# Kernel tuning notes

Hardware: AMD Instinct MI355X
Metric: run time of the kernel (lower is better)

Reference implementation:

```python
import jax, jax.numpy as jnp
import numpy as np

TOP_K = 1024  # init top_k


def setup_inputs() -> dict:
    key = jax.random.key(0)
    ks = jax.random.split(key, 11)
    B, S, D, H = 8, 1024, 1024, 4096
    s = 0.02
    return {
        "inputs": jax.random.normal(ks[0], (B, S, D), jnp.float32),
        "up_w": jax.random.normal(ks[1], (H, D), jnp.float32) * s,
        "up_b": jax.random.normal(ks[2], (H,), jnp.float32) * s,
        "gate_w1": jax.random.normal(ks[3], (H, D), jnp.float32) * s,
        "gate_b1": jax.random.normal(ks[4], (H,), jnp.float32) * s,
        "gate_w2": jax.random.normal(ks[5], (H, H), jnp.float32) * s,
        "gate_b2": jax.random.normal(ks[6], (H,), jnp.float32) * s,
        "mod_w": jax.random.normal(ks[7], (H, D), jnp.float32) * s,
        "mod_b": jax.random.normal(ks[8], (H,), jnp.float32) * s,
        "down_w": jax.random.normal(ks[9], (D, H), jnp.float32) * s,
        "down_b": jax.random.normal(ks[10], (D,), jnp.float32) * s,
    }


def reference(inputs, up_w, up_b, gate_w1, gate_b1, gate_w2, gate_b2,
              mod_w, mod_b, down_w, down_b):
    B, S, D = inputs.shape
    H = up_w.shape[0]
    # gate: Linear -> ReLU -> Linear, scores [B,S,H]
    scores = jax.nn.relu(jnp.einsum('bsd,hd->bsh', inputs, gate_w1) + gate_b1)
    scores = jnp.einsum('bsh,gh->bsg', scores, gate_w2) + gate_b2
    flat_scores = scores.reshape(B, S * H)
    k = min(TOP_K * S, S * H)
    _, flat_idx = jax.lax.top_k(flat_scores, k)          # [B,k]
    hidden_idx = flat_idx % H                            # [B,k]
    # scatter writes mod.weight[h] at row h -> duplicates harmless -> boolean mask
    batch_idx = jnp.broadcast_to(jnp.arange(B)[:, None], (B, k))
    mask = jnp.zeros((B, H), bool).at[batch_idx, hidden_idx].set(True)
    # per-batch modified weights/bias (materialized like torch repeat+index_put)
    w = jnp.where(mask[:, :, None], mod_w[None], up_w[None])   # [B,H,D]
    b = jnp.where(mask, mod_b[None], up_b[None])               # [B,H]
    h = jnp.einsum('bsd,bhd->bsh', inputs, w) + b[:, None, :]
    h = jax.nn.silu(h)
    # dropout p=0.0 (eval) -> identity
    return jnp.einsum('bsh,dh->bsd', h, down_w) + down_b
```

## Files before the change

kernel.cpp:

```cpp
#include <hip/hip_runtime.h>
#include <cstdint>

typedef __attribute__((ext_vector_type(8))) short short8;
typedef __attribute__((ext_vector_type(4))) float floatx4;
typedef unsigned int uint32;

typedef const void __attribute__((address_space(1)))* gcptr;
typedef void __attribute__((address_space(3)))* lptr;

constexpr int Bn = 8, Sn = 1024, Dn = 1024, Hn = 4096;
constexpr uint32 KTOP = 1024u * 1024u;
constexpr uint32 SKBASE = 0xBB000000u;
constexpr uint32 EMAX = (1u << 27) - 1u;
constexpr uint32 WLO = 3645;
constexpr uint32 WHI = 4157;
constexpr uint32 CAP = 1u << 20;

constexpr size_t NX  = (size_t)Bn * Sn * Dn;
constexpr size_t NW1 = (size_t)Hn * Dn;
constexpr size_t NW2 = (size_t)Hn * Hn;
constexpr size_t NRS = (size_t)Bn * Sn * Hn;

constexpr size_t OFF_XH   = 0;
constexpr size_t OFF_XL   = OFF_XH  + 2 * NX;
constexpr size_t OFF_W1H  = OFF_XL  + 2 * NX;
constexpr size_t OFF_W1L  = OFF_W1H + 2 * NW1;
constexpr size_t OFF_W2H  = OFF_W1L + 2 * NW1;
constexpr size_t OFF_W2L  = OFF_W2H + 2 * NW2;
constexpr size_t OFF_RSH  = OFF_W2L + 2 * NW2;
constexpr size_t OFF_RSL  = OFF_RSH + 2 * NRS;
constexpr size_t OFF_HIST = OFF_RSL + 2 * NRS;
constexpr size_t OFF_HIST2= OFF_HIST + (size_t)Bn * 8192 * 4;
constexpr size_t OFF_HMAX = OFF_HIST2+ (size_t)Bn * 16384 * 4;
constexpr size_t OFF_META = OFF_HMAX + (size_t)Bn * Hn * 4;
constexpr size_t OFF_BSEL = OFF_META + 4096;
constexpr size_t OFF_MASK = OFF_BSEL + (size_t)Bn * Hn * 4;
constexpr size_t WS_SMALL = OFF_MASK + (size_t)Bn * Hn * 4;
constexpr size_t ZERO_BYTES = OFF_BSEL - OFF_HIST;
constexpr size_t OFF_BUF  = OFF_XL;

__device__ __forceinline__ ushort f2bf(float f) {
  uint32 u = __float_as_uint(f);
  u += 0x7fffu + ((u >> 16) & 1u);
  return (ushort)(u >> 16);
}
__device__ __forceinline__ float bf2f(ushort h) {
  return __uint_as_float(((uint32)h) << 16);
}
__device__ __forceinline__ uint32 skey(float v) {
  uint32 u = __float_as_uint(v);
  return (u & 0x80000000u) ? ~u : (u | 0x80000000u);
}
__device__ __forceinline__ uint32 ekey(uint32 key) {
  if (key <= SKBASE) return 0u;
  uint32 d = key - SKBASE;
  return d > EMAX ? EMAX : d;
}
__device__ __forceinline__ void g2l(const ushort* src, ushort* dst) {
  __builtin_amdgcn_global_load_lds((gcptr)src, (lptr)dst, 16, 0, 0);
}
__device__ __forceinline__ void stage_tile(ushort* lds, const ushort* gbase, int ldg, int tid) {
  const int w = tid >> 6;
  const int c0 = tid, c1 = tid + 256;
  g2l(gbase + (size_t)(c0 >> 2) * ldg + (c0 & 3) * 8, lds + (size_t)(w * 64) * 8);
  g2l(gbase + (size_t)(c1 >> 2) * ldg + (c1 & 3) * 8, lds + (size_t)(256 + w * 64) * 8);
}
__device__ __forceinline__ void stage_tile_sel(ushort* lds, const ushort* upw,
                                               const ushort* modw, const uint32* bm,
                                               int n0, int k0, int ldg, int tid) {
  const int w = tid >> 6;
  const int c0 = tid, c1 = tid + 256;
  const int r0 = n0 + (c0 >> 2), r1 = n0 + (c1 >> 2);
  const ushort* s0 = (bm[r0] ? modw : upw) + (size_t)r0 * ldg + k0 + (c0 & 3) * 8;
  const ushort* s1 = (bm[r1] ? modw : upw) + (size_t)r1 * ldg + k0 + (c1 & 3) * 8;
  g2l(s0, lds + (size_t)(w * 64) * 8);
  g2l(s1, lds + (size_t)(256 + w * 64) * 8);
}

__global__ __launch_bounds__(256) void cvt_split_k(const float4* __restrict__ x,
                                                   ushort* __restrict__ hi,
                                                   ushort* __restrict__ lo, int n4) {
  int stride = gridDim.x * 256;
  for (int i = blockIdx.x * 256 + threadIdx.x; i < n4; i += stride) {
    float4 v = x[i];
    ushort h0 = f2bf(v.x), h1 = f2bf(v.y), h2 = f2bf(v.z), h3 = f2bf(v.w);
    ushort4 hv; hv.x = h0; hv.y = h1; hv.z = h2; hv.w = h3;
    *(ushort4*)(hi + (size_t)i * 4) = hv;
    ushort4 lv;
    lv.x = f2bf(v.x - bf2f(h0)); lv.y = f2bf(v.y - bf2f(h1));
    lv.z = f2bf(v.z - bf2f(h2)); lv.w = f2bf(v.w - bf2f(h3));
    *(ushort4*)(lo + (size_t)i * 4) = lv;
  }
}
__global__ __launch_bounds__(256) void cvt_single_k(const float4* __restrict__ x,
                                                    ushort* __restrict__ hi, int n4) {
  int stride = gridDim.x * 256;
  for (int i = blockIdx.x * 256 + threadIdx.x; i < n4; i += stride) {
    float4 v = x[i];
    ushort4 hv; hv.x = f2bf(v.x); hv.y = f2bf(v.y); hv.z = f2bf(v.z); hv.w = f2bf(v.w);
    *(ushort4*)(hi + (size_t)i * 4) = hv;
  }
}
__global__ __launch_bounds__(256) void zero_out_k(float* __restrict__ o, int n) {
  int i = blockIdx.x * 256 + threadIdx.x;
  if (i < n) o[i] = 0.f;
}

constexpr int EPI_RELU = 0;
constexpr int EPI_SCORE = 1;
constexpr int EPI_SILU = 2;
constexpr int EPI_F32 = 3;

template <bool SPLIT, bool SELB, int EPI>
__global__ __launch_bounds__(256, SPLIT ? 3 : 2) void gemm_bt(
    const ushort* __restrict__ Ah, const ushort* __restrict__ Al,
    const ushort* __restrict__ Bh, const ushort* __restrict__ Bl,
    const uint32* __restrict__ bmask,
    int N, int K, long long a_bs, long long o_bs, long long bias_bs,
    const float* __restrict__ bias,
    void* __restrict__ outp, void* __restrict__ out2p,
    uint32* __restrict__ hist, uint32* __restrict__ hmax,
    uint32* __restrict__ buf, uint32* __restrict__ cnt) {
  static_assert(EPI != EPI_SCORE || SPLIT, "score path is split");
  __shared__ __align__(16) ushort lds[SPLIT ? 16384 : 8192];
  ushort* As = lds;
  ushort* Bs = lds + (SPLIT ? 8192 : 4096);

  const int tid = threadIdx.x;
  const int w = tid >> 6, l = tid & 63;
  const int wm = (w >> 1) << 6, wn = (w & 1) << 6;
  const int lm = l & 15, lq = l >> 4;
  const int m0 = blockIdx.y << 7, n0 = blockIdx.x << 7;
  const int z = blockIdx.z;

  const ushort* pAh = Ah + (size_t)z * a_bs + (size_t)m0 * K;
  const ushort* pAl = SPLIT ? Al + (size_t)z * a_bs + (size_t)m0 * K : nullptr;
  const ushort* pBh = SELB ? nullptr : Bh + (size_t)n0 * K;
  const ushort* pBl = (SPLIT && !SELB) ? Bl + (size_t)n0 * K : nullptr;
  const uint32* bm = SELB ? bmask + (size_t)z * Hn : nullptr;

  floatx4 acc[4][4];
#pragma unroll
  for (int i = 0; i < 4; i++)
#pragma unroll
    for (int j = 0; j < 4; j++) acc[i][j] = floatx4{0.f, 0.f, 0.f, 0.f};

  for (int k0 = 0; k0 < K; k0 += 32) {
    stage_tile(As, pAh + k0, K, tid);
    if constexpr (SELB)
      stage_tile_sel(Bs, Bh, Bl, bm, n0, k0, K, tid);
    else
      stage_tile(Bs, pBh + k0, K, tid);
    if constexpr (SPLIT) {
      stage_tile(As + 4096, pAl + k0, K, tid);
      stage_tile(Bs + 4096, pBl + k0, K, tid);
    }
    __syncthreads();
    short8 afh[4], bfh[4];
#pragma unroll
    for (int i = 0; i < 4; i++)
      afh[i] = *(const short8*)&As[(wm + i * 16 + lm) * 32 + lq * 8];
#pragma unroll
    for (int i = 0; i < 4; i++)
      bfh[i] = *(const short8*)&Bs[(wn + i * 16 + lm) * 32 + lq * 8];
#pragma unroll
    for (int mi = 0; mi < 4; mi++)
#pragma unroll
      for (int ni = 0; ni < 4; ni++)
        acc[mi][ni] = __builtin_amdgcn_mfma_f32_16x16x32_bf16(afh[mi], bfh[ni], acc[mi][ni], 0, 0, 0);
    if constexpr (SPLIT) {
      {
        short8 afl[4];
#pragma unroll
        for (int i = 0; i < 4; i++)
          afl[i] = *(const short8*)&As[4096 + (wm + i * 16 + lm) * 32 + lq * 8];
#pragma unroll
        for (int mi = 0; mi < 4; mi++)
#pragma unroll
          for (int ni = 0; ni < 4; ni++)
            acc[mi][ni] = __builtin_amdgcn_mfma_f32_16x16x32_bf16(afl[mi], bfh[ni], acc[mi][ni], 0, 0, 0);
      }
      {
        short8 bfl[4];
#pragma unroll
        for (int i = 0; i < 4; i++)
          bfl[i] = *(const short8*)&Bs[4096 + (wn + i * 16 + lm) * 32 + lq * 8];
#pragma unroll
        for (int mi = 0; mi < 4; mi++)
#pragma unroll
          for (int ni = 0; ni < 4; ni++)
            acc[mi][ni] = __builtin_amdgcn_mfma_f32_16x16x32_bf16(afh[mi], bfl[ni], acc[mi][ni], 0, 0, 0);
      }
    }
    __syncthreads();
  }

  if constexpr (EPI == EPI_RELU) {
    ushort* rh = (ushort*)outp;
    ushort* rl = (ushort*)out2p;
#pragma unroll
    for (int mi = 0; mi < 4; mi++)
#pragma unroll
      for (int ni = 0; ni < 4; ni++) {
        int gm = m0 + wm + mi * 16 + lq * 4;
        int gn = n0 + wn + ni * 16 + lm;
        float bnv = bias[gn];
#pragma unroll
        for (int r = 0; r < 4; r++) {
          float v = fmaxf(acc[mi][ni][r] + bnv, 0.f);
          ushort h = f2bf(v);
          size_t o = (size_t)(gm + r) * N + gn;
          rh[o] = h;
          rl[o] = f2bf(v - bf2f(h));
        }
      }
  } else if constexpr (EPI == EPI_SILU) {
    ushort* o = (ushort*)outp + (size_t)z * o_bs;
    const float* bb = bias + (size_t)z * bias_bs;
#pragma unroll
    for (int mi = 0; mi < 4; mi++)
#pragma unroll
      for (int ni = 0; ni < 4; ni++) {
        int gm = m0 + wm + mi * 16 + lq * 4;
        int gn = n0 + wn + ni * 16 + lm;
        float bnv = bb[gn];
#pragma unroll
        for (int r = 0; r < 4; r++) {
          float v = acc[mi][ni][r] + bnv;
          float s = v / (1.f + __expf(-v));
          o[(size_t)(gm + r) * N + gn] = f2bf(s);
        }
      }
  } else if constexpr (EPI == EPI_F32) {
    float* o = (float*)outp;
#pragma unroll
    for (int mi = 0; mi < 4; mi++)
#pragma unroll
      for (int ni = 0; ni < 4; ni++) {
        int gm = m0 + wm + mi * 16 + lq * 4;
        int gn = n0 + wn + ni * 16 + lm;
        float bnv = bias[gn];
#pragma unroll
        for (int r = 0; r < 4; r++)
          o[(size_t)(gm + r) * N + gn] = acc[mi][ni][r] + bnv;
      }
  } else {
    uint32* hs = (uint32*)lds;
    for (int i = tid; i < 8192; i += 256) hs[i] = 0;
    __syncthreads();
    const int batch = m0 >> 10;
    uint32 cntl = 0;
#pragma unroll
    for (int ni = 0; ni < 4; ni++) {
      int gn = n0 + wn + ni * 16 + lm;
      float bnv = bias[gn];
      float vmax = -3.4e38f;
#pragma unroll
      for (int mi = 0; mi < 4; mi++) {
#pragma unroll
        for (int r = 0; r < 4; r++) {
          float v = acc[mi][ni][r] + bnv;
          uint32 e = ekey(skey(v));
          uint32 bk = e >> 14;
          atomicAdd(&hs[bk], 1u);
          if (bk >= WLO && bk <= WHI) cntl++;
          vmax = fmaxf(vmax, v);
        }
      }
      atomicMax(&hmax[batch * Hn + gn], skey(vmax));
    }
    __syncthreads();
    for (int i = tid; i < 8192; i += 256) {
      uint32 c = hs[i];
      if (c) atomicAdd(&hist[batch * 8192 + i], c);
    }
    __syncthreads();
    hs[tid] = cntl;
    __syncthreads();
    if (tid == 0) {
      uint32 run = 0;
      for (int i = 0; i < 256; i++) { uint32 t = hs[i]; hs[i] = run; run += t; }
      hs[256] = atomicAdd(&cnt[batch], run);
    }
    __syncthreads();
    uint32 off = hs[256] + hs[tid];
    uint32* bb = buf + (size_t)batch * CAP;
#pragma unroll
    for (int ni = 0; ni < 4; ni++) {
      int gn = n0 + wn + ni * 16 + lm;
      float bnv = bias[gn];
#pragma unroll
      for (int mi = 0; mi < 4; mi++) {
#pragma unroll
        for (int r = 0; r < 4; r++) {
          float v = acc[mi][ni][r] + bnv;
          uint32 e = ekey(skey(v));
          uint32 bk = e >> 14;
          if (bk >= WLO && bk <= WHI) {
            if (off < CAP) bb[off] = e;
            off++;
          }
        }
      }
    }
  }
}

__global__ __launch_bounds__(256) void select1_k(const uint32* __restrict__ hist,
                                                 uint32* __restrict__ meta) {
  int b = blockIdx.x;
  const uint32* h = hist + b * 8192;
  __shared__ uint32 ps[256];
  uint32 s = 0;
  int base = threadIdx.x * 32;
  for (int i = 0; i < 32; i++) s += h[base + i];
  ps[threadIdx.x] = s;
  __syncthreads();
  if (threadIdx.x == 0) {
    uint32 cum = 0, need = 1;
    int j = 0;
    for (int c = 255; c >= 0; c--) {
      if (cum + ps[c] >= KTOP) {
        for (int i = c * 32 + 31;; i--) {
          uint32 hv = h[i];
          if (cum + hv >= KTOP) { j = i; need = KTOP - cum; break; }
          cum += hv;
        }
        break;
      }
      cum += ps[c];
    }
    meta[8 + b] = (uint32)j;
    meta[16 + b] = need;
    meta[b] = SKBASE + ((uint32)j << 14);
  }
}

__global__ __launch_bounds__(256) void refine_buf_k(const uint32* __restrict__ buf,
                                                    const uint32* __restrict__ meta,
                                                    uint32* __restrict__ hist2) {
  const uint32* cnt = meta + 32;
  size_t stride = (size_t)gridDim.x * 256;
  for (int b = 0; b < Bn; b++) {
    uint32 n = cnt[b] < CAP ? cnt[b] : CAP;
    uint32 j = meta[8 + b];
    const uint32* bb = buf + (size_t)b * CAP;
    for (size_t i = (size_t)blockIdx.x * 256 + threadIdx.x; i < n; i += stride) {
      uint32 e = bb[i];
      if ((e >> 14) == j) atomicAdd(&hist2[(size_t)b * 16384 + (e & 0x3FFFu)], 1u);
    }
  }
}

__global__ __launch_bounds__(256) void select2_k(const uint32* __restrict__ hist2,
                                                 uint32* __restrict__ meta) {
  int b = blockIdx.x;
  const uint32* h2 = hist2 + (size_t)b * 16384;
  __shared__ uint32 ps[256];
  uint32 s = 0;
  const uint32* p = h2 + (size_t)threadIdx.x * 64;
  for (int i = 0; i < 64; i += 4) {
    uint4 v = *(const uint4*)(p + i);
    s += v.x + v.y + v.z + v.w;
  }
  ps[threadIdx.x] = s;
  __syncthreads();
  if (threadIdx.x == 0) {
    uint32 j = meta[8 + b];
    uint32 valid = (j >= WLO && j <= WHI && meta[32 + b] <= CAP) ? 1u : 0u;
    if (valid) {
      uint32 need = meta[16 + b];
      uint32 cum = 0;
      int c = 255;
      for (; c > 0; c--) {
        if (cum + ps[c] >= need) break;
        cum += ps[c];
      }
      uint32 rem = 0;
      for (int i = 63; i >= 0; i--) {
        uint32 hv = h2[c * 64 + i];
        if (cum + hv >= need) { rem = (uint32)(c * 64 + i); break; }
        cum += hv;
      }
      meta[b] = SKBASE + (j << 14) + rem;
    }
  }
}

__global__ __launch_bounds__(256) void mask_k(const uint32* __restrict__ hmax,
                                              const uint32* __restrict__ meta,
                                              const float* __restrict__ modb,
                                              const float* __restrict__ upb,
                                              uint32* __restrict__ mask,
                                              float* __restrict__ bsel) {
  int i = blockIdx.x * 256 + threadIdx.x;
  int b = i >> 12, h = i & 4095;
  bool m = hmax[i] >= meta[b];
  mask[i] = m ? 1u : 0u;
  bsel[i] = m ? modb[h] : upb[h];
}

extern "C" void kernel_launch(void* const* d_in, const int* in_sizes, int n_in,
                              void* d_out, int out_size, void* d_ws, size_t ws_size,
                              hipStream_t stream) {
  (void)in_sizes; (void)n_in;
  const float* x    = (const float*)d_in[0];
  const float* up_w = (const float*)d_in[1];
  const float* up_b = (const float*)d_in[2];
  const float* g_w1 = (const float*)d_in[3];
  const float* g_b1 = (const float*)d_in[4];
  const float* g_w2 = (const float*)d_in[5];
  const float* g_b2 = (const float*)d_in[6];
  const float* mod_w= (const float*)d_in[7];
  const float* mod_b= (const float*)d_in[8];
  const float* dw   = (const float*)d_in[9];
  const float* db   = (const float*)d_in[10];
  float* out = (float*)d_out;

  if (ws_size < WS_SMALL) {
    zero_out_k<<<(out_size + 255) / 256, 256, 0, stream>>>(out, out_size);
    return;
  }

  char* ws = (char*)d_ws;
  ushort* XH  = (ushort*)(ws + OFF_XH);
  ushort* XL  = (ushort*)(ws + OFF_XL);
  ushort* W1H = (ushort*)(ws + OFF_W1H);
  ushort* W1L = (ushort*)(ws + OFF_W1L);
  ushort* W2H = (ushort*)(ws + OFF_W2H);
  ushort* W2L = (ushort*)(ws + OFF_W2L);
  ushort* RSH = (ushort*)(ws + OFF_RSH);
  ushort* RSL = (ushort*)(ws + OFF_RSL);
  uint32* HIST = (uint32*)(ws + OFF_HIST);
  uint32* HIST2= (uint32*)(ws + OFF_HIST2);
  uint32* HMAX = (uint32*)(ws + OFF_HMAX);
  uint32* META = (uint32*)(ws + OFF_META);
  float*  BSEL = (float*)(ws + OFF_BSEL);
  uint32* MASK = (uint32*)(ws + OFF_MASK);
  uint32* BUF  = (uint32*)(ws + OFF_BUF);
  ushort* UPW  = W1H;
  ushort* MODW = W1L;
  ushort* DWNW = XL;
  ushort* HBUF = RSH;

  hipMemsetAsync(ws + OFF_HIST, 0, ZERO_BYTES, stream);

  cvt_split_k<<<1024, 256, 0, stream>>>((const float4*)x, XH, XL, (int)(NX / 4));
  cvt_split_k<<<1024, 256, 0, stream>>>((const float4*)g_w1, W1H, W1L, (int)(NW1 / 4));
  cvt_split_k<<<2048, 256, 0, stream>>>((const float4*)g_w2, W2H, W2L, (int)(NW2 / 4));

  gemm_bt<true, false, EPI_RELU><<<dim3(Hn / 128, (Bn * Sn) / 128, 1), 256, 0, stream>>>(
      XH, XL, W1H, W1L, nullptr, Hn, Dn, 0, 0, 0, g_b1, RSH, RSL,
      nullptr, nullptr, nullptr, nullptr);
  gemm_bt<true, false, EPI_SCORE><<<dim3(Hn / 128, (Bn * Sn) / 128, 1), 256, 0, stream>>>(
      RSH, RSL, W2H, W2L, nullptr, Hn, Hn, 0, 0, 0, g_b2, nullptr, nullptr,
      HIST, HMAX, BUF, META + 32);
  select1_k<<<Bn, 256, 0, stream>>>(HIST, META);
  refine_buf_k<<<512, 256, 0, stream>>>(BUF, META, HIST2);
  select2_k<<<Bn, 256, 0, stream>>>(HIST2, META);
  mask_k<<<(Bn * Hn) / 256, 256, 0, stream>>>(HMAX, META, mod_b, up_b, MASK, BSEL);

  cvt_single_k<<<1024, 256, 0, stream>>>((const float4*)up_w, UPW, (int)(NW1 / 4));
  cvt_single_k<<<1024, 256, 0, stream>>>((const float4*)mod_w, MODW, (int)(NW1 / 4));
  cvt_single_k<<<1024, 256, 0, stream>>>((const float4*)dw, DWNW, (int)(NW1 / 4));

  gemm_bt<false, true, EPI_SILU><<<dim3(Hn / 128, Sn / 128, Bn), 256, 0, stream>>>(
      XH, nullptr, UPW, MODW, MASK, Hn, Dn,
      (long long)Sn * Dn, (long long)Sn * Hn, (long long)Hn,
      BSEL, HBUF, nullptr, nullptr, nullptr, nullptr, nullptr);
  gemm_bt<false, false, EPI_F32><<<dim3(Dn / 128, (Bn * Sn) / 128, 1), 256, 0, stream>>>(
      HBUF, nullptr, DWNW, nullptr, nullptr, Dn, Hn, 0, 0, 0, db, out, nullptr,
      nullptr, nullptr, nullptr, nullptr);
}
```

Measured before the change: 1.541 ms.

## Add 256x256 double-buffered pipelined GEMM kernel for split-bf16 gate GEMMs

Replaces the 128x128 split-precision gemm_bt for the two gate GEMMs with a new 512-thread 256x256 tile kernel. It double-buffers LDS, interleaves global-to-LDS staging with MFMA phases using explicit barriers, vmcnt waits and setprio, and swizzles LDS to avoid bank conflicts. The aim is more operand reuse per loaded byte and latency hiding for the dominant gate GEMMs. The cost is heavier register pressure (32 accumulators per lane), fragile hand-tuned waitcnt counts, and a larger histogram-epilogue tile.

```diff
diff --git a/kernel.cpp b/kernel.cpp
--- a/kernel.cpp
+++ b/kernel.cpp
@@ -121,7 +121,6 @@
     void* __restrict__ outp, void* __restrict__ out2p,
     uint32* __restrict__ hist, uint32* __restrict__ hmax,
     uint32* __restrict__ buf, uint32* __restrict__ cnt) {
-  static_assert(EPI != EPI_SCORE || SPLIT, "score path is split");
   __shared__ __align__(16) ushort lds[SPLIT ? 16384 : 8192];
   ushort* As = lds;
   ushort* Bs = lds + (SPLIT ? 8192 : 4096);
@@ -195,26 +194,7 @@
     __syncthreads();
   }
 
-  if constexpr (EPI == EPI_RELU) {
-    ushort* rh = (ushort*)outp;
-    ushort* rl = (ushort*)out2p;
-#pragma unroll
-    for (int mi = 0; mi < 4; mi++)
-#pragma unroll
-      for (int ni = 0; ni < 4; ni++) {
-        int gm = m0 + wm + mi * 16 + lq * 4;
-        int gn = n0 + wn + ni * 16 + lm;
-        float bnv = bias[gn];
-#pragma unroll
-        for (int r = 0; r < 4; r++) {
-          float v = fmaxf(acc[mi][ni][r] + bnv, 0.f);
-          ushort h = f2bf(v);
-          size_t o = (size_t)(gm + r) * N + gn;
-          rh[o] = h;
-          rl[o] = f2bf(v - bf2f(h));
-        }
-      }
-  } else if constexpr (EPI == EPI_SILU) {
+  if constexpr (EPI == EPI_SILU) {
     ushort* o = (ushort*)outp + (size_t)z * o_bs;
     const float* bb = bias + (size_t)z * bias_bs;
 #pragma unroll
@@ -244,19 +224,190 @@
         for (int r = 0; r < 4; r++)
           o[(size_t)(gm + r) * N + gn] = acc[mi][ni][r] + bnv;
       }
+  }
+}
+
+#define LGKM0 do { asm volatile("s_waitcnt lgkmcnt(0)" ::: "memory"); \
+                   __builtin_amdgcn_sched_barrier(0); } while (0)
+
+__device__ __forceinline__ short8 fragld(const ushort* S, int r, int swz) {
+  return *(const short8*)&S[r * 32 + swz];
+}
+__device__ __forceinline__ void stage256(ushort* d, const ushort* g,
+                                         size_t soff0, size_t soff1, int dbase) {
+  g2l(g + soff0, d + dbase);
+  g2l(g + soff1, d + dbase + 4096);
+}
+__device__ __forceinline__ void mfma_block(floatx4 (&acc)[8][4], const short8 (&af)[4],
+                                           int mi0, const short8 (&bf)[4]) {
+#pragma unroll
+  for (int mi = 0; mi < 4; mi++)
+#pragma unroll
+    for (int ni = 0; ni < 4; ni++)
+      acc[mi0 + mi][ni] =
+          __builtin_amdgcn_mfma_f32_16x16x32_bf16(af[mi], bf[ni], acc[mi0 + mi][ni], 0, 0, 0);
+}
+
+template <bool ST>
+__device__ __forceinline__ void kstep256(
+    floatx4 (&acc)[8][4], ushort (&lds)[2][4][8192], int p,
+    const ushort* nA0, const ushort* nB0, const ushort* nA1, const ushort* nB1,
+    size_t soff0, size_t soff1, int dbase, int swz, int lm, int wrow, int wcol) {
+  const ushort* AhS = &lds[p][0][0];
+  const ushort* BhS = &lds[p][1][0];
+  const ushort* AlS = &lds[p][2][0];
+  const ushort* BlS = &lds[p][3][0];
+  ushort* dA0 = &lds[p ^ 1][0][0];
+  ushort* dB0 = &lds[p ^ 1][1][0];
+  ushort* dA1 = &lds[p ^ 1][2][0];
+  ushort* dB1 = &lds[p ^ 1][3][0];
+
+  short8 afh0[4], afh1[4], bfh[4];
+#pragma unroll
+  for (int i = 0; i < 4; i++) afh0[i] = fragld(AhS, wrow + i * 16 + lm, swz);
+#pragma unroll
+  for (int i = 0; i < 4; i++) bfh[i] = fragld(BhS, wcol + i * 16 + lm, swz);
+  if constexpr (ST) stage256(dA0, nA0, soff0, soff1, dbase);
+  __builtin_amdgcn_s_barrier();
+  LGKM0;
+  __builtin_amdgcn_s_setprio(1);
+  mfma_block(acc, afh0, 0, bfh);
+  __builtin_amdgcn_s_setprio(0);
+  __builtin_amdgcn_s_barrier();
+#pragma unroll
+  for (int i = 0; i < 4; i++) afh1[i] = fragld(AhS, wrow + 64 + i * 16 + lm, swz);
+  if constexpr (ST) stage256(dB0, nB0, soff0, soff1, dbase);
+  __builtin_amdgcn_s_barrier();
+  LGKM0;
+  __builtin_amdgcn_s_setprio(1);
+  mfma_block(acc, afh1, 4, bfh);
+  __builtin_amdgcn_s_setprio(0);
+  if constexpr (ST) asm volatile("s_waitcnt vmcnt(6)" ::: "memory");
+  else              asm volatile("s_waitcnt vmcnt(2)" ::: "memory");
+  __builtin_amdgcn_s_barrier();
+  {
+    short8 afl[4];
+#pragma unroll
+    for (int i = 0; i < 4; i++) afl[i] = fragld(AlS, wrow + i * 16 + lm, swz);
+    if constexpr (ST) stage256(dA1, nA1, soff0, soff1, dbase);
+    __builtin_amdgcn_s_barrier();
+    LGKM0;
+    __builtin_amdgcn_s_setprio(1);
+    mfma_block(acc, afl, 0, bfh);
+    __builtin_amdgcn_s_setprio(0);
+    __builtin_amdgcn_s_barrier();
+  }
+  {
+    short8 afl[4];
+#pragma unroll
+    for (int i = 0; i < 4; i++) afl[i] = fragld(AlS, wrow + 64 + i * 16 + lm, swz);
+    if constexpr (ST) stage256(dB1, nB1, soff0, soff1, dbase);
+    __builtin_amdgcn_s_barrier();
+    LGKM0;
+    __builtin_amdgcn_s_setprio(1);
+    mfma_block(acc, afl, 4, bfh);
+    __builtin_amdgcn_s_setprio(0);
+    if constexpr (ST) asm volatile("s_waitcnt vmcnt(8)" ::: "memory");
+    else              asm volatile("s_waitcnt vmcnt(0)" ::: "memory");
+    __builtin_amdgcn_s_barrier();
+  }
+  {
+    short8 bfl[4];
+#pragma unroll
+    for (int i = 0; i < 4; i++) bfl[i] = fragld(BlS, wcol + i * 16 + lm, swz);
+    __builtin_amdgcn_s_barrier();
+    LGKM0;
+    __builtin_amdgcn_s_setprio(1);
+    mfma_block(acc, afh0, 0, bfl);
+    mfma_block(acc, afh1, 4, bfl);
+    __builtin_amdgcn_s_setprio(0);
+    if constexpr (ST) asm volatile("s_waitcnt vmcnt(4)" ::: "memory");
+    __builtin_amdgcn_s_barrier();
+  }
+}
+
+template <int EPI>
+__global__ __launch_bounds__(512, 2) void gemm256(
+    const ushort* __restrict__ Ah, const ushort* __restrict__ Al,
+    const ushort* __restrict__ Bh, const ushort* __restrict__ Bl,
+    int N, int K, const float* __restrict__ bias,
+    ushort* __restrict__ outh, ushort* __restrict__ outl,
+    uint32* __restrict__ hist, uint32* __restrict__ hmax,
+    uint32* __restrict__ buf, uint32* __restrict__ cnt) {
+  static_assert(EPI == EPI_RELU || EPI == EPI_SCORE, "gemm256 handles G1/G2 only");
+  __shared__ __align__(16) ushort lds[2][4][8192];
+  const int tid = threadIdx.x;
+  const int l = tid & 63, w = tid >> 6;
+  const int lm = l & 15, lq = l >> 4;
+  const int swz = (lq ^ ((lm >> 1) & 3)) << 3;
+  const int wrow = (w >> 2) << 7, wcol = (w & 3) << 6;
+  const int m0 = blockIdx.y << 8, n0 = blockIdx.x << 8;
+
+  const int cg = ((l & 3) ^ ((l >> 3) & 3)) << 3;
+  const int r0 = (w << 4) + (l >> 2);
+  const size_t soff0 = (size_t)r0 * K + cg;
+  const size_t soff1 = soff0 + (size_t)128 * K;
+  const int dbase = w << 9;
+
+  const ushort* pA0 = Ah + (size_t)m0 * K;
+  const ushort* pA1 = Al + (size_t)m0 * K;
+  const ushort* pB0 = Bh + (size_t)n0 * K;
+  const ushort* pB1 = Bl + (size_t)n0 * K;
+
+  floatx4 acc[8][4];
+#pragma unroll
+  for (int i = 0; i < 8; i++)
+#pragma unroll
+    for (int j = 0; j < 4; j++) acc[i][j] = floatx4{0.f, 0.f, 0.f, 0.f};
+
+  stage256(&lds[0][0][0], pA0, soff0, soff1, dbase);
+  stage256(&lds[0][1][0], pB0, soff0, soff1, dbase);
+  stage256(&lds[0][2][0], pA1, soff0, soff1, dbase);
+  stage256(&lds[0][3][0], pB1, soff0, soff1, dbase);
+  asm volatile("s_waitcnt vmcnt(4)" ::: "memory");
+  __builtin_amdgcn_s_barrier();
+
+  const int nk = K >> 5;
+  int T = 0;
+  for (; T < nk - 1; ++T) {
+    const int ko = (T + 1) << 5;
+    kstep256<true>(acc, lds, T & 1, pA0 + ko, pB0 + ko, pA1 + ko, pB1 + ko,
+                   soff0, soff1, dbase, swz, lm, wrow, wcol);
+  }
+  kstep256<false>(acc, lds, T & 1, pA0, pB0, pA1, pB1,
+                  soff0, soff1, dbase, swz, lm, wrow, wcol);
+
+  if constexpr (EPI == EPI_RELU) {
+#pragma unroll
+    for (int mi = 0; mi < 8; mi++)
+#pragma unroll
+      for (int ni = 0; ni < 4; ni++) {
+        const int gm = m0 + wrow + mi * 16 + lq * 4;
+        const int gn = n0 + wcol + ni * 16 + lm;
+        const float bnv = bias[gn];
+#pragma unroll
+        for (int r = 0; r < 4; r++) {
+          float v = fmaxf(acc[mi][ni][r] + bnv, 0.f);
+          ushort h = f2bf(v);
+          size_t o = (size_t)(gm + r) * N + gn;
+          outh[o] = h;
+          outl[o] = f2bf(v - bf2f(h));
+        }
+      }
   } else {
-    uint32* hs = (uint32*)lds;
-    for (int i = tid; i < 8192; i += 256) hs[i] = 0;
+    __syncthreads();
+    uint32* hs = (uint32*)&lds[0][0][0];
+    for (int i = tid; i < 8192; i += 512) hs[i] = 0;
     __syncthreads();
     const int batch = m0 >> 10;
     uint32 cntl = 0;
 #pragma unroll
     for (int ni = 0; ni < 4; ni++) {
-      int gn = n0 + wn + ni * 16 + lm;
-      float bnv = bias[gn];
+      const int gn = n0 + wcol + ni * 16 + lm;
+      const float bnv = bias[gn];
       float vmax = -3.4e38f;
 #pragma unroll
-      for (int mi = 0; mi < 4; mi++) {
+      for (int mi = 0; mi < 8; mi++) {
 #pragma unroll
         for (int r = 0; r < 4; r++) {
           float v = acc[mi][ni][r] + bnv;
@@ -270,7 +421,7 @@
       atomicMax(&hmax[batch * Hn + gn], skey(vmax));
     }
     __syncthreads();
-    for (int i = tid; i < 8192; i += 256) {
+    for (int i = tid; i < 8192; i += 512) {
       uint32 c = hs[i];
       if (c) atomicAdd(&hist[batch * 8192 + i], c);
     }
@@ -279,18 +430,18 @@
     __syncthreads();
     if (tid == 0) {
       uint32 run = 0;
-      for (int i = 0; i < 256; i++) { uint32 t = hs[i]; hs[i] = run; run += t; }
-      hs[256] = atomicAdd(&cnt[batch], run);
-    }
-    __syncthreads();
-    uint32 off = hs[256] + hs[tid];
+      for (int i = 0; i < 512; i++) { uint32 t = hs[i]; hs[i] = run; run += t; }
+      hs[512] = atomicAdd(&cnt[batch], run);
+    }
+    __syncthreads();
+    uint32 off = hs[512] + hs[tid];
     uint32* bb = buf + (size_t)batch * CAP;
 #pragma unroll
     for (int ni = 0; ni < 4; ni++) {
-      int gn = n0 + wn + ni * 16 + lm;
-      float bnv = bias[gn];
-#pragma unroll
-      for (int mi = 0; mi < 4; mi++) {
+      const int gn = n0 + wcol + ni * 16 + lm;
+      const float bnv = bias[gn];
+#pragma unroll
+      for (int mi = 0; mi < 8; mi++) {
 #pragma unroll
         for (int r = 0; r < 4; r++) {
           float v = acc[mi][ni][r] + bnv;
@@ -449,12 +600,11 @@
   cvt_split_k<<<1024, 256, 0, stream>>>((const float4*)g_w1, W1H, W1L, (int)(NW1 / 4));
   cvt_split_k<<<2048, 256, 0, stream>>>((const float4*)g_w2, W2H, W2L, (int)(NW2 / 4));
 
-  gemm_bt<true, false, EPI_RELU><<<dim3(Hn / 128, (Bn * Sn) / 128, 1), 256, 0, stream>>>(
-      XH, XL, W1H, W1L, nullptr, Hn, Dn, 0, 0, 0, g_b1, RSH, RSL,
-      nullptr, nullptr, nullptr, nullptr);
-  gemm_bt<true, false, EPI_SCORE><<<dim3(Hn / 128, (Bn * Sn) / 128, 1), 256, 0, stream>>>(
-      RSH, RSL, W2H, W2L, nullptr, Hn, Hn, 0, 0, 0, g_b2, nullptr, nullptr,
-      HIST, HMAX, BUF, META + 32);
+  gemm256<EPI_RELU><<<dim3(Hn / 256, (Bn * Sn) / 256), 512, 0, stream>>>(
+      XH, XL, W1H, W1L, Hn, Dn, g_b1, RSH, RSL, nullptr, nullptr, nullptr, nullptr);
+  gemm256<EPI_SCORE><<<dim3(Hn / 256, (Bn * Sn) / 256), 512, 0, stream>>>(
+      RSH, RSL, W2H, W2L, Hn, Hn, g_b2, nullptr, nullptr, HIST, HMAX, BUF, META + 32);
+
   select1_k<<<Bn, 256, 0, stream>>>(HIST, META);
   refine_buf_k<<<512, 256, 0, stream>>>(BUF, META, HIST2);
   select2_k<<<Bn, 256, 0, stream>>>(HIST2, META);
```

After: 1.246 ms. -19.1%, faster.
